# Optimization experiments

Measured on AMD Instinct MI355X. Metric: run time of the kernel, lower is better.

## Reference

```python
import jax, jax.numpy as jnp
import numpy as np


def setup_inputs() -> dict:
    key = jax.random.key(0)
    ks = jax.random.split(key, 5)
    B, S, H, I, E = 4, 2048, 1024, 4096, 8
    scale_in = 1.0 / np.sqrt(H)
    scale_mid = 1.0 / np.sqrt(I)
    return {
        "x": jax.random.normal(ks[0], (B, S, H), dtype=jnp.float32),
        "w_gate": jax.random.normal(ks[1], (H, E), dtype=jnp.float32) * scale_in,
        "w1": jax.random.normal(ks[2], (E, H, I), dtype=jnp.float32) * scale_in,
        "w2": jax.random.normal(ks[3], (E, I, H), dtype=jnp.float32) * scale_mid,
        "w3": jax.random.normal(ks[4], (E, H, I), dtype=jnp.float32) * scale_in,
        "num_experts_per_tok": 2,
    }


def reference(x, w_gate, w1, w2, w3, num_experts_per_tok):
    """MoE with top-k routing and SwiGLU experts (Mixtral-style).

    x: [B, S, H]; w_gate: [H, E]; w1/w3: [E, H, I]; w2: [E, I, H].
    Returns [B, S, H]. Matches torch module output (aux_loss is a side
    attribute in the original, not returned).
    """
    B, S, H = x.shape
    E = w_gate.shape[1]
    K = num_experts_per_tok
    xf = x.reshape(-1, H)                           # [T, H]

    logits = xf @ w_gate                            # [T, E]
    probs = jax.nn.softmax(logits, axis=-1)
    topk_probs, topk_idx = jax.lax.top_k(probs, K)  # [T, K]
    topk_probs = topk_probs / topk_probs.sum(axis=-1, keepdims=True)

    # Per-token per-expert combine weight: sum over k of renormalized top-k
    # probs mapped back to expert slots. [T, E]
    comb = jnp.sum(jax.nn.one_hot(topk_idx, E, dtype=xf.dtype)
                   * topk_probs[..., None], axis=1)

    out = jnp.zeros_like(xf)
    for e in range(E):  # small fixed loop over experts
        hidden = jax.nn.silu(xf @ w1[e]) * (xf @ w3[e])  # [T, I]
        out = out + (hidden @ w2[e]) * comb[:, e:e + 1]
    return out.reshape(B, S, H)
```

## Files before the change

### kernel.cpp

```cpp
#include <hip/hip_runtime.h>

typedef unsigned short u16;
typedef __attribute__((ext_vector_type(4))) float f32x4;
typedef __attribute__((ext_vector_type(8))) short s16x8;

#define T_TOK 8192
#define HD    1024
#define ID    4096
#define NE    8
#define AK    (T_TOK * 2)
#define APAD  (AK + 256)
#define MTMAX 72

#define BAR()   __builtin_amdgcn_s_barrier()
#define SB0()   __builtin_amdgcn_sched_barrier(0)
#define PRIO1() __builtin_amdgcn_s_setprio(1)
#define PRIO0() __builtin_amdgcn_s_setprio(0)
#define WAITV6() asm volatile("s_waitcnt vmcnt(6)" ::: "memory")
#define WAITV8() asm volatile("s_waitcnt vmcnt(8)" ::: "memory")
#define LGKM0()  do { asm volatile("s_waitcnt lgkmcnt(0)" ::: "memory"); SB0(); } while (0)

__device__ __forceinline__ u16 f2bf(float f) {
  unsigned u = __builtin_bit_cast(unsigned, f);
  u += 0x7FFFu + ((u >> 16) & 1u);
  return (u16)(u >> 16);
}

__device__ __forceinline__ float bf2f(u16 v) {
  unsigned u = (unsigned)v << 16;
  return __builtin_bit_cast(float, u);
}

__device__ __forceinline__ void gld16(u16* lds, const u16* g) {
  __builtin_amdgcn_global_load_lds(
      (const __attribute__((address_space(1))) unsigned int*)g,
      (__attribute__((address_space(3))) unsigned int*)lds, 16, 0, 0);
}


__global__ void k_init(int* counts) {
  if (threadIdx.x < NE) counts[threadIdx.x] = 0;
}

__global__ void k_offsets(const int* __restrict__ counts, int* offs, int* cursors,
                          int* __restrict__ tiles, int* __restrict__ ntile) {
  if (threadIdx.x == 0) {
    int s = 0;
    for (int e = 0; e < NE; ++e) { offs[e] = s; s += counts[e]; }
    offs[NE] = s;
    int nt = 0;
    for (int e = 0; e < NE; ++e)
      for (int m0 = 0; m0 < counts[e]; m0 += 256)
        tiles[nt++] = (e << 16) | (m0 >> 8);
    ntile[0] = nt;
    for (int i = nt; i < MTMAX; ++i) tiles[i] = 0;
  }
  if (threadIdx.x < NE) cursors[threadIdx.x] = 0;
}

__global__ __launch_bounds__(256) void k_scatter(
    const int* __restrict__ tidx, const int* __restrict__ offs,
    int* cursors, int* __restrict__ list, int* __restrict__ pos) {
  int idx = blockIdx.x * 256 + threadIdx.x;
  if (idx >= AK) return;
  int e = tidx[idx];
  int p = atomicAdd(&cursors[e], 1);
  int a = offs[e] + p;
  list[a] = idx >> 1;
  pos[idx] = a;
}


#define NBP_T13 4096
#define NBP_RTR 2048

__global__ __launch_bounds__(256) void k_prep(
    const float* __restrict__ x, const float* __restrict__ wg,
    const float* __restrict__ w1, const float* __restrict__ w3,
    u16* __restrict__ xb, u16* __restrict__ w13b,
    int* __restrict__ tidx, float* __restrict__ tw, int* __restrict__ counts) {
  __shared__ char smem[256 * 72 * 2];
  int bid = blockIdx.x, t = threadIdx.x;

  if (bid < NBP_T13) {
    u16 (*tile)[72] = (u16(*)[72])smem;
    int bx = bid & 63;
    int by = (bid >> 6) & 3;
    int bz = bid >> 8;
    int which = bz >> 3, e = bz & 7;
    const float* in = (which ? w3 : w1) + (size_t)e * HD * ID;
    int r0 = by * 256, c0 = bx * 64;
    int rr = t >> 4, cc4 = (t & 15) * 4;
#pragma unroll
    for (int i = 0; i < 16; ++i) {
      int r = i * 16 + rr;
      float4 v = *(const float4*)&in[(size_t)(r0 + r) * ID + c0 + cc4];
      ushort4 bv;
      bv.x = f2bf(v.x); bv.y = f2bf(v.y); bv.z = f2bf(v.z); bv.w = f2bf(v.w);
      *(ushort4*)&tile[r][cc4] = bv;
    }
    __syncthreads();
    int w = t >> 6, c = t & 63;
    int gc = c0 + c;
    int orow = ((gc >> 4) << 5) + which * 16 + (gc & 15);
    u16* obase = w13b + ((size_t)e * 2 * ID + orow) * HD + r0 + w * 64;
#pragma unroll
    for (int j = 0; j < 8; ++j) {
      s16x8 o;
#pragma unroll
      for (int q = 0; q < 8; ++q) o[q] = (short)tile[w * 64 + j * 8 + q][c];
      *(s16x8*)&obase[j * 8] = o;
    }
    return;
  }
  {
    float* wgs = (float*)smem;
    int blockR = bid - NBP_T13;
    for (int i = t; i < NE * HD; i += 256) {
      int h = i >> 3, e = i & 7;
      wgs[e * HD + h] = wg[i];
    }
    __syncthreads();
    int lane = t & 63, wid = t >> 6;
    int tok = blockR * 4 + wid;
    const float* xr = x + (size_t)tok * HD;
    u16* xo = xb + (size_t)tok * HD;
    double acc[NE];
#pragma unroll
    for (int e = 0; e < NE; ++e) acc[e] = 0.0;
    for (int i = 0; i < HD / 64; ++i) {
      float xv = xr[lane + i * 64];
      xo[lane + i * 64] = f2bf(xv);
#pragma unroll
      for (int e = 0; e < NE; ++e)
        acc[e] += (double)xv * (double)wgs[e * HD + lane + i * 64];
    }
#pragma unroll
    for (int e = 0; e < NE; ++e)
      for (int s = 32; s >= 1; s >>= 1) acc[e] += __shfl_xor(acc[e], s, 64);
    int e0 = 0; double m0 = acc[0];
    for (int e = 1; e < NE; ++e) if (acc[e] > m0) { m0 = acc[e]; e0 = e; }
    int e1 = -1; double m1 = -1e300;
    for (int e = 0; e < NE; ++e) if (e != e0 && acc[e] > m1) { m1 = acc[e]; e1 = e; }
    if (lane == 0) {
      double d = exp(m1 - m0);
      tidx[tok * 2] = e0; tidx[tok * 2 + 1] = e1;
      tw[tok * 2] = (float)(1.0 / (1.0 + d));
      tw[tok * 2 + 1] = (float)(d / (1.0 + d));
      atomicAdd(&counts[e0], 1);
      atomicAdd(&counts[e1], 1);
    }
  }
}


#define GEMM_CORE(NTK, NITER) \
  int wr = wid >> 2, wc = wid & 3; \
  int lane15 = lane & 15, lq = lane >> 4, sw8 = lane15 & 7; \
  f32x4 acc[8][4]; \
  _Pragma("unroll") for (int m = 0; m < 8; ++m) \
    _Pragma("unroll") for (int n = 0; n < 4; ++n) acc[m][n] = (f32x4){0.f,0.f,0.f,0.f}; \
  auto stgA = [&](int bb, int h, int kt) { \
    gld16(&As[bb][(h*128 + 0*64 + wid*8) * 64], gA[h*2+0] + kt*64); \
    gld16(&As[bb][(h*128 + 1*64 + wid*8) * 64], gA[h*2+1] + kt*64); }; \
  auto stgB = [&](int bb, int h, int kt) { \
    gld16(&Bs[bb][(h*128 + 0*64 + wid*8) * 64], gB[h*2+0] + kt*64); \
    gld16(&Bs[bb][(h*128 + 1*64 + wid*8) * 64], gB[h*2+1] + kt*64); }; \
  s16x8 a[4][2], b[4][2]; \
  auto rdA = [&](int bb, int mh) { \
    _Pragma("unroll") for (int mm = 0; mm < 4; ++mm) \
      _Pragma("unroll") for (int kk = 0; kk < 2; ++kk) \
        a[mm][kk] = *(const s16x8*)&As[bb][(mh*128 + wr*64 + mm*16 + lane15)*64 + (((kk*4+lq)^sw8)*8)]; }; \
  auto rdB = [&](int bb, int fh) { \
    _Pragma("unroll") for (int ff = 0; ff < 2; ++ff) \
      _Pragma("unroll") for (int kk = 0; kk < 2; ++kk) \
        b[fh*2+ff][kk] = *(const s16x8*)&Bs[bb][(fh*128 + wc*32 + ff*16 + lane15)*64 + (((kk*4+lq)^sw8)*8)]; }; \
  auto mf = [&](int mh, int fh) { \
    _Pragma("unroll") for (int kk = 0; kk < 2; ++kk) \
      _Pragma("unroll") for (int mm = 0; mm < 4; ++mm) \
        _Pragma("unroll") for (int ff = 0; ff < 2; ++ff) \
          acc[mh*4+mm][fh*2+ff] = __builtin_amdgcn_mfma_f32_16x16x32_bf16(a[mm][kk], b[fh*2+ff][kk], acc[mh*4+mm][fh*2+ff], 0, 0, 0); }; \
   \
  stgA(0,0,0); stgB(0,0,0); stgA(0,1,0); stgB(0,1,0); stgA(1,0,1); stgB(1,0,1); \
  WAITV8(); BAR(); SB0(); \
  for (int i = 0; i < (NITER); ++i) { \
    int ku2 = (2*i+2) & ((NTK)-1), ku3 = (2*i+3) & ((NTK)-1); \
     rdA(0,0); rdB(0,0); stgA(1,1,2*i+1); WAITV6(); BAR(); LGKM0(); PRIO1(); mf(0,0); PRIO0(); BAR(); SB0(); \
     rdB(0,1); stgB(1,1,2*i+1); BAR(); LGKM0(); PRIO1(); mf(0,1); PRIO0(); BAR(); SB0(); \
     rdA(0,1); stgA(0,0,ku2); BAR(); LGKM0(); PRIO1(); mf(1,0); PRIO0(); BAR(); SB0(); \
     stgB(0,0,ku2); WAITV8(); BAR(); PRIO1(); mf(1,1); PRIO0(); BAR(); SB0(); \
     rdA(1,0); rdB(1,0); stgA(0,1,ku2); WAITV6(); BAR(); LGKM0(); PRIO1(); mf(0,0); PRIO0(); BAR(); SB0(); \
     rdB(1,1); stgB(0,1,ku2); BAR(); LGKM0(); PRIO1(); mf(0,1); PRIO0(); BAR(); SB0(); \
     rdA(1,1); stgA(1,0,ku3); BAR(); LGKM0(); PRIO1(); mf(1,0); PRIO0(); BAR(); SB0(); \
     stgB(1,0,ku3); WAITV8(); BAR(); PRIO1(); mf(1,1); PRIO0(); BAR(); SB0(); \
  }


__global__ __launch_bounds__(512, 1) void k_gemm1(
    const u16* __restrict__ xb, const u16* __restrict__ w13b,
    const int* __restrict__ list, const int* __restrict__ offs,
    const int* __restrict__ tiles, const int* __restrict__ ntile,
    u16* __restrict__ hidden,
    const float* __restrict__ w2, u16* __restrict__ w2b) {
  __shared__ u16 As[2][256 * 64];
  __shared__ u16 Bs[2][256 * 64];
  int tid = threadIdx.x, lane = tid & 63, wid = tid >> 6;

  if (blockIdx.y >= MTMAX) {
    u16 (*tile)[64] = (u16(*)[64])&As[0][0];
    int flat = (blockIdx.y - MTMAX) * 32 + blockIdx.x;
    int bx = flat & 15, by = (flat >> 4) & 15, e2 = flat >> 8;
    const float* in = w2 + (size_t)e2 * ID * HD;
    u16* outp = w2b + (size_t)e2 * HD * ID;
    int r0 = by * 256, c0 = bx * 64;
    int rr = tid >> 4, cc4 = (tid & 15) * 4;
#pragma unroll
    for (int i = 0; i < 8; ++i) {
      int r = i * 32 + rr;
      float4 v = *(const float4*)&in[(size_t)(r0 + r) * HD + c0 + cc4];
      ushort4 bv;
      bv.x = f2bf(v.x); bv.y = f2bf(v.y); bv.z = f2bf(v.z); bv.w = f2bf(v.w);
      *(ushort4*)&tile[r][cc4] = bv;
    }
    __syncthreads();
    int w = tid >> 6, c = tid & 63;
    u16* obase = outp + (size_t)(c0 + c) * ID + r0 + w * 32;
#pragma unroll
    for (int j = 0; j < 4; ++j) {
      s16x8 o;
#pragma unroll
      for (int q = 0; q < 8; ++q) o[q] = (short)tile[w * 32 + j * 8 + q][c];
      *(s16x8*)&obase[j * 8] = o;
    }
    return;
  }

  int ti = blockIdx.y;
  if (ti >= ntile[0]) return;
  int packed = tiles[ti];
  int e = packed >> 16;
  int m0 = (packed & 0xFFFF) << 8;
  int aoff = offs[e];
  int cnt = offs[e + 1] - aoff;
  int n0 = blockIdx.x * 256;

  int l8 = lane >> 3, c8 = lane & 7;
  int csrc = (c8 ^ l8) * 8;

  const u16* gA[4]; const u16* gB[4];
#pragma unroll
  for (int h = 0; h < 2; ++h)
#pragma unroll
    for (int c = 0; c < 2; ++c) {
      int row = h * 128 + c * 64 + wid * 8 + l8;
      int rr = m0 + row; if (rr > cnt - 1) rr = cnt - 1;
      gA[h*2+c] = xb + (size_t)list[aoff + rr] * HD + csrc;
      gB[h*2+c] = w13b + ((size_t)e * 2 * ID + n0 + row) * HD + csrc;
    }

  GEMM_CORE(HD / 64, HD / 128)

  u16 (*Ls)[132] = (u16(*)[132])&As[0][0];
  BAR();
#pragma unroll
  for (int mh = 0; mh < 2; ++mh)
#pragma unroll
    for (int mm = 0; mm < 4; ++mm)
#pragma unroll
      for (int j = 0; j < 4; ++j) {
        int rl = mh * 128 + wr * 64 + mm * 16 + lq * 4 + j;
#pragma unroll
        for (int p = 0; p < 2; ++p) {
          float v1 = acc[mh*4+mm][2*p][j];
          float v3 = acc[mh*4+mm][2*p+1][j];
          float s = v1 / (1.0f + __expf(-v1));
          Ls[rl][p * 64 + wc * 16 + lane15] = f2bf(s * v3);
        }
      }
  BAR();
#pragma unroll
  for (int ps = 0; ps < 8; ++ps) {
    int r = ps * 32 + (tid >> 4);
    int grow = m0 + r;
    if (grow < cnt) {
      int cl = (tid & 15) * 8;
      *(s16x8*)&hidden[(size_t)(aoff + grow) * ID + (n0 >> 1) + cl] =
          *(const s16x8*)&Ls[r][cl];
    }
  }
}

__global__ __launch_bounds__(512, 1) void k_gemm2(
    const u16* __restrict__ hidden, const u16* __restrict__ w2b,
    const int* __restrict__ offs, const int* __restrict__ tiles,
    const int* __restrict__ ntile,
    u16* __restrict__ yp0, u16* __restrict__ yp3) {
  int ti = blockIdx.y;
  if (ti >= ntile[0]) return;
  int packed = tiles[ti];
  int e = packed >> 16;
  int m0 = (packed & 0xFFFF) << 8;
  int aoff = offs[e];
  int cnt = offs[e + 1] - aoff;
  int n0 = (blockIdx.x & 3) * 256;
  int kidx = blockIdx.x >> 2;
  int kc = kidx * 1024;

  __shared__ u16 As[2][256 * 64];
  __shared__ u16 Bs[2][256 * 64];

  int tid = threadIdx.x, lane = tid & 63, wid = tid >> 6;
  int l8 = lane >> 3, c8 = lane & 7;
  int csrc = (c8 ^ l8) * 8;

  const u16* gA[4]; const u16* gB[4];
#pragma unroll
  for (int h = 0; h < 2; ++h)
#pragma unroll
    for (int c = 0; c < 2; ++c) {
      int row = h * 128 + c * 64 + wid * 8 + l8;
      gA[h*2+c] = hidden + (size_t)(aoff + m0 + row) * ID + kc + csrc;
      gB[h*2+c] = w2b + ((size_t)e * HD + n0 + row) * ID + kc + csrc;
    }

  GEMM_CORE(1024 / 64, 1024 / 128)

  u16* yp = (kidx < 3) ? yp0 + (size_t)kidx * AK * HD : yp3;
  u16 (*Ls)[132] = (u16(*)[132])&As[0][0];
#pragma unroll
  for (int half = 0; half < 2; ++half) {
    BAR();
#pragma unroll
    for (int mh = 0; mh < 2; ++mh)
#pragma unroll
      for (int mm = 0; mm < 4; ++mm)
#pragma unroll
        for (int j = 0; j < 4; ++j) {
          int rl = mh * 128 + wr * 64 + mm * 16 + lq * 4 + j;
#pragma unroll
          for (int fo = 0; fo < 2; ++fo) {
            int f = half * 2 + fo;
            Ls[rl][wc * 32 + fo * 16 + lane15] = f2bf(acc[mh*4+mm][f][j]);
          }
        }
    BAR();
#pragma unroll
    for (int ps = 0; ps < 8; ++ps) {
      int r = ps * 32 + (tid >> 4);
      int grow = m0 + r;
      if (grow < cnt) {
        int cl = (tid & 15) * 8;
        *(s16x8*)&yp[(size_t)(aoff + grow) * HD + n0 + half * 128 + cl] =
            *(const s16x8*)&Ls[r][cl];
      }
    }
  }
}

__global__ __launch_bounds__(256) void k_combine(
    const u16* __restrict__ yp0, const u16* __restrict__ yp3,
    const int* __restrict__ pos, const float* __restrict__ tw,
    float* __restrict__ out) {
  int t = blockIdx.x;
  int c = threadIdx.x * 4;
  int a0 = pos[t * 2], a1 = pos[t * 2 + 1];
  float w0 = tw[t * 2], w1 = tw[t * 2 + 1];
  float s0[4] = {0.f, 0.f, 0.f, 0.f}, s1[4] = {0.f, 0.f, 0.f, 0.f};
#pragma unroll
  for (int k = 0; k < 4; ++k) {
    const u16* yp = (k < 3) ? yp0 + (size_t)k * AK * HD : yp3;
    ushort4 v0 = *(const ushort4*)&yp[(size_t)a0 * HD + c];
    ushort4 v1 = *(const ushort4*)&yp[(size_t)a1 * HD + c];
    s0[0] += bf2f(v0.x); s0[1] += bf2f(v0.y); s0[2] += bf2f(v0.z); s0[3] += bf2f(v0.w);
    s1[0] += bf2f(v1.x); s1[1] += bf2f(v1.y); s1[2] += bf2f(v1.z); s1[3] += bf2f(v1.w);
  }
  float4 o;
  o.x = w0 * s0[0] + w1 * s1[0];
  o.y = w0 * s0[1] + w1 * s1[1];
  o.z = w0 * s0[2] + w1 * s1[2];
  o.w = w0 * s0[3] + w1 * s1[3];
  *(float4*)&out[(size_t)t * HD + c] = o;
}


extern "C" void kernel_launch(void* const* d_in, const int* in_sizes, int n_in,
                              void* d_out, int out_size, void* d_ws, size_t ws_size,
                              hipStream_t stream) {
  const float* x  = (const float*)d_in[0];
  const float* wg = (const float*)d_in[1];
  const float* w1 = (const float*)d_in[2];
  const float* w2 = (const float*)d_in[3];
  const float* w3 = (const float*)d_in[4];

  char* p = (char*)d_ws;
  auto alloc = [&](size_t bytes) {
    char* r = p;
    p += (bytes + 255) & ~(size_t)255;
    return r;
  };
  u16*   xb      = (u16*)alloc((size_t)T_TOK * HD * 2);
  u16*   w13b    = (u16*)alloc((size_t)NE * 2 * ID * HD * 2);
  u16*   w2b     = (u16*)alloc((size_t)NE * HD * ID * 2);
  u16*   hidden  = (u16*)alloc((size_t)APAD * ID * 2);
  u16*   yp3     = (u16*)alloc((size_t)AK * HD * 2);
  int*   tidx    = (int*)alloc(AK * 4);
  float* tw      = (float*)alloc(AK * 4);
  int*   list    = (int*)alloc(AK * 4);
  int*   pos     = (int*)alloc(AK * 4);
  int*   counts  = (int*)alloc(64);
  int*   offs    = (int*)alloc(64);
  int*   cursors = (int*)alloc(64);
  int*   tiles   = (int*)alloc(MTMAX * 4);
  int*   ntile   = (int*)alloc(64);
  (void)ws_size; (void)in_sizes; (void)n_in; (void)out_size;

  u16* yp0 = w13b;

  k_init<<<1, 64, 0, stream>>>(counts);
  k_prep<<<NBP_T13 + NBP_RTR, 256, 0, stream>>>(
      x, wg, w1, w3, xb, w13b, tidx, tw, counts);
  k_offsets<<<1, 64, 0, stream>>>(counts, offs, cursors, tiles, ntile);
  k_scatter<<<AK / 256, 256, 0, stream>>>(tidx, offs, cursors, list, pos);

  dim3 gg1(2 * ID / 256, MTMAX + 64, 1);
  k_gemm1<<<gg1, 512, 0, stream>>>(xb, w13b, list, offs, tiles, ntile, hidden,
                                   w2, w2b);
  dim3 gg2(16, MTMAX, 1);
  k_gemm2<<<gg2, 512, 0, stream>>>(hidden, w2b, offs, tiles, ntile, yp0, yp3);
  k_combine<<<T_TOK, 256, 0, stream>>>(yp0, yp3, pos, tw, (float*)d_out);
}
```

Measured before the change: 870.0 us.

## Remove offsets kernel; decode expert tiles in-kernel and remap block order

Drops the single-thread k_init and k_offsets kernels. The counts buffer is zeroed with a memset, and the scatter and GEMM kernels now compute expert offsets and tile decoding directly from counts. The GEMM grids become 1D, with a remapped block index that interleaves work across groups of eight consecutive blocks, presumably to spread expert and N tiles differently across compute units and XCDs. This removes two serialized launches, but each GEMM block now runs a small loop over counts.

```diff
diff --git a/kernel.cpp b/kernel.cpp
--- a/kernel.cpp
+++ b/kernel.cpp
@@ -37,35 +37,30 @@
       (__attribute__((address_space(3))) unsigned int*)lds, 16, 0, 0);
 }
 
-
-__global__ void k_init(int* counts) {
-  if (threadIdx.x < NE) counts[threadIdx.x] = 0;
-}
-
-__global__ void k_offsets(const int* __restrict__ counts, int* offs, int* cursors,
-                          int* __restrict__ tiles, int* __restrict__ ntile) {
-  if (threadIdx.x == 0) {
-    int s = 0;
-    for (int e = 0; e < NE; ++e) { offs[e] = s; s += counts[e]; }
-    offs[NE] = s;
-    int nt = 0;
-    for (int e = 0; e < NE; ++e)
-      for (int m0 = 0; m0 < counts[e]; m0 += 256)
-        tiles[nt++] = (e << 16) | (m0 >> 8);
-    ntile[0] = nt;
-    for (int i = nt; i < MTMAX; ++i) tiles[i] = 0;
-  }
-  if (threadIdx.x < NE) cursors[threadIdx.x] = 0;
-}
+__device__ __forceinline__ int decode_tile(const int* __restrict__ counts,
+                                           int ti, int& e, int& m0,
+                                           int& aoff, int& cnt) {
+  int s = 0;
+  for (int ee = 0; ee < NE; ++ee) {
+    int c = counts[ee];
+    int nt = (c + 255) >> 8;
+    if (ti < nt) { e = ee; m0 = ti << 8; aoff = s; cnt = c; return 1; }
+    ti -= nt; s += c;
+  }
+  return 0;
+}
+
 
 __global__ __launch_bounds__(256) void k_scatter(
-    const int* __restrict__ tidx, const int* __restrict__ offs,
+    const int* __restrict__ tidx, const int* __restrict__ counts,
     int* cursors, int* __restrict__ list, int* __restrict__ pos) {
   int idx = blockIdx.x * 256 + threadIdx.x;
   if (idx >= AK) return;
   int e = tidx[idx];
+  int off = 0;
+  for (int ee = 0; ee < NE; ++ee) off += (ee < e) ? counts[ee] : 0;
   int p = atomicAdd(&cursors[e], 1);
-  int a = offs[e] + p;
+  int a = off + p;
   list[a] = idx >> 1;
   pos[idx] = a;
 }
@@ -195,20 +190,22 @@
      stgB(1,0,ku3); WAITV8(); BAR(); PRIO1(); mf(1,1); PRIO0(); BAR(); SB0(); \
   }
 
+#define NGEMM1 (32 * MTMAX)
+#define NGEMM2 (16 * MTMAX)
 
 __global__ __launch_bounds__(512, 1) void k_gemm1(
     const u16* __restrict__ xb, const u16* __restrict__ w13b,
-    const int* __restrict__ list, const int* __restrict__ offs,
-    const int* __restrict__ tiles, const int* __restrict__ ntile,
+    const int* __restrict__ list, const int* __restrict__ counts,
     u16* __restrict__ hidden,
     const float* __restrict__ w2, u16* __restrict__ w2b) {
   __shared__ u16 As[2][256 * 64];
   __shared__ u16 Bs[2][256 * 64];
   int tid = threadIdx.x, lane = tid & 63, wid = tid >> 6;
-
-  if (blockIdx.y >= MTMAX) {
+  int bid = blockIdx.x;
+
+  if (bid >= NGEMM1) {
     u16 (*tile)[64] = (u16(*)[64])&As[0][0];
-    int flat = (blockIdx.y - MTMAX) * 32 + blockIdx.x;
+    int flat = bid - NGEMM1;
     int bx = flat & 15, by = (flat >> 4) & 15, e2 = flat >> 8;
     const float* in = w2 + (size_t)e2 * ID * HD;
     u16* outp = w2b + (size_t)e2 * HD * ID;
@@ -235,14 +232,12 @@
     return;
   }
 
-  int ti = blockIdx.y;
-  if (ti >= ntile[0]) return;
-  int packed = tiles[ti];
-  int e = packed >> 16;
-  int m0 = (packed & 0xFFFF) << 8;
-  int aoff = offs[e];
-  int cnt = offs[e + 1] - aoff;
-  int n0 = blockIdx.x * 256;
+  int work = (bid & 7) * (NGEMM1 / 8) + (bid >> 3);
+  int nx = work / MTMAX;
+  int ti = work % MTMAX;
+  int e, m0, aoff, cnt;
+  if (!decode_tile(counts, ti, e, m0, aoff, cnt)) return;
+  int n0 = nx * 256;
 
   int l8 = lane >> 3, c8 = lane & 7;
   int csrc = (c8 ^ l8) * 8;
@@ -292,18 +287,16 @@
 
 __global__ __launch_bounds__(512, 1) void k_gemm2(
     const u16* __restrict__ hidden, const u16* __restrict__ w2b,
-    const int* __restrict__ offs, const int* __restrict__ tiles,
-    const int* __restrict__ ntile,
+    const int* __restrict__ counts,
     u16* __restrict__ yp0, u16* __restrict__ yp3) {
-  int ti = blockIdx.y;
-  if (ti >= ntile[0]) return;
-  int packed = tiles[ti];
-  int e = packed >> 16;
-  int m0 = (packed & 0xFFFF) << 8;
-  int aoff = offs[e];
-  int cnt = offs[e + 1] - aoff;
-  int n0 = (blockIdx.x & 3) * 256;
-  int kidx = blockIdx.x >> 2;
+  int bid = blockIdx.x;
+  int work = (bid & 7) * (NGEMM2 / 8) + (bid >> 3);
+  int px = work / MTMAX;
+  int ti = work % MTMAX;
+  int e, m0, aoff, cnt;
+  if (!decode_tile(counts, ti, e, m0, aoff, cnt)) return;
+  int n0 = (px & 3) * 256;
+  int kidx = px >> 2;
   int kc = kidx * 1024;
 
   __shared__ u16 As[2][256 * 64];
@@ -408,24 +401,18 @@
   int*   list    = (int*)alloc(AK * 4);
   int*   pos     = (int*)alloc(AK * 4);
   int*   counts  = (int*)alloc(64);
-  int*   offs    = (int*)alloc(64);
-  int*   cursors = (int*)alloc(64);
-  int*   tiles   = (int*)alloc(MTMAX * 4);
-  int*   ntile   = (int*)alloc(64);
+  int*   cursors = counts + 8;
   (void)ws_size; (void)in_sizes; (void)n_in; (void)out_size;
 
   u16* yp0 = w13b;
 
-  k_init<<<1, 64, 0, stream>>>(counts);
+  hipMemsetAsync(counts, 0, 64, stream);
   k_prep<<<NBP_T13 + NBP_RTR, 256, 0, stream>>>(
       x, wg, w1, w3, xb, w13b, tidx, tw, counts);
-  k_offsets<<<1, 64, 0, stream>>>(counts, offs, cursors, tiles, ntile);
-  k_scatter<<<AK / 256, 256, 0, stream>>>(tidx, offs, cursors, list, pos);
-
-  dim3 gg1(2 * ID / 256, MTMAX + 64, 1);
-  k_gemm1<<<gg1, 512, 0, stream>>>(xb, w13b, list, offs, tiles, ntile, hidden,
-                                   w2, w2b);
-  dim3 gg2(16, MTMAX, 1);
-  k_gemm2<<<gg2, 512, 0, stream>>>(hidden, w2b, offs, tiles, ntile, yp0, yp3);
+  k_scatter<<<AK / 256, 256, 0, stream>>>(tidx, counts, cursors, list, pos);
+
+  k_gemm1<<<NGEMM1 + 2048, 512, 0, stream>>>(xb, w13b, list, counts, hidden,
+                                             w2, w2b);
+  k_gemm2<<<NGEMM2, 512, 0, stream>>>(hidden, w2b, counts, yp0, yp3);
   k_combine<<<T_TOK, 256, 0, stream>>>(yp0, yp3, pos, tw, (float*)d_out);
 }
```

Measured after the change: 861.8 us. Within noise of the previous version (-0.9%).
